# Kernel optimization log

Measured on AMD Instinct MI355X. Metric: run time of the kernel, lower is better.

Reference implementation:

```python
import jax, jax.numpy as jnp
import numpy as np

# sizes
N, B, NPG = 8192, 8, 1024          # total nodes, graphs, nodes per graph (equal-size graphs)
D, H, DH, L = 256, 8, 32, 2        # hidden, heads, head dim, layers
IN_C, OUT_D, E, DFF = 128, 64, 262144, 512
EPS = 1e-5


def setup_inputs() -> dict:
    key = jax.random.key(0)
    ks = jax.random.split(key, 20)
    p = lambda i, shp: jax.random.normal(ks[i], shp, jnp.float32) * 0.05
    return dict(
        x=jax.random.normal(ks[0], (N, IN_C), jnp.float32),
        edge_index=jax.random.randint(ks[1], (2, E), 0, N),
        batch=jnp.arange(N, dtype=jnp.int32) // NPG,  # sorted, equal-size graphs
        w_in=p(2, (D, IN_C)), b_in=p(3, (D,)),
        sage_wl=p(4, (L, D, D)), sage_bl=p(5, (L, D)), sage_wr=p(6, (L, D, D)),
        attn_iw=p(7, (L, 3 * D, D)), attn_ib=p(8, (L, 3 * D)),
        attn_ow=p(9, (L, D, D)), attn_ob=p(10, (L, D)),
        n1_w=jnp.ones((L, D)), n1_b=jnp.zeros((L, D)),
        n2_w=jnp.ones((L, D)), n2_b=jnp.zeros((L, D)),
        n3_w=jnp.ones((L, D)), n3_b=jnp.zeros((L, D)),
        mlp_w1=p(11, (L, DFF, D)), mlp_b1=p(12, (L, DFF)),
        mlp_w2=p(13, (L, D, DFF)), mlp_b2=p(14, (L, D)),
        bn_w=jnp.ones((L, D)), bn_b=jnp.zeros((L, D)),
        w_out=p(15, (OUT_D, D)), b_out=p(16, (OUT_D,)),
    )


def _bn(h, w, b):
    # BatchNorm1d over nodes (training-mode batch statistics, biased var)
    m = h.mean(0)
    v = jnp.mean((h - m) ** 2, axis=0)
    return (h - m) * jax.lax.rsqrt(v + EPS) * w + b


def _forward(x, edge_index, batch, w_in, b_in, sage_wl, sage_bl, sage_wr,
             attn_iw, attn_ib, attn_ow, attn_ob, n1_w, n1_b, n2_w, n2_b,
             n3_w, n3_b, mlp_w1, mlp_b1, mlp_w2, mlp_b2, bn_w, bn_b, w_out, b_out):
    src, dst = edge_index[0], edge_index[1]
    deg = jax.ops.segment_sum(jnp.ones((E,), jnp.float32), dst, num_segments=N)
    inv_deg = (1.0 / jnp.clip(deg, 1.0))[:, None]
    scale = 1.0 / np.sqrt(DH)

    h = x @ w_in.T + b_in  # in_proj Linear  [N, D]
    for l in range(L):
        # --- GPSConv: local SAGEConv (mean aggr) + residual + norm1 ---
        agg = jax.ops.segment_sum(h[src], dst, num_segments=N) * inv_deg
        loc = agg @ sage_wl[l].T + sage_bl[l] + h @ sage_wr[l].T
        loc = _bn(loc + h, n1_w[l], n1_b[l])
        # --- GPSConv: dense per-graph multi-head self-attention + residual + norm2 ---
        hd = h.reshape(B, NPG, D)  # to_dense_batch (no padding: equal graph sizes)
        qkv = hd @ attn_iw[l].T + attn_ib[l]  # [B, n, 3D]
        q, k, v = jnp.split(qkv, 3, axis=-1)
        sh = lambda t: t.reshape(B, NPG, H, DH).transpose(0, 2, 1, 3)  # [B, H, n, DH]
        a = jax.nn.softmax(jnp.einsum('bhqd,bhkd->bhqk', sh(q) * scale, sh(k)), axis=-1)
        o = jnp.einsum('bhqk,bhkd->bhqd', a, sh(v)).transpose(0, 2, 1, 3).reshape(B, NPG, D)
        o = (o @ attn_ow[l].T + attn_ob[l]).reshape(N, D)
        glob = _bn(o + h, n2_w[l], n2_b[l])
        # --- GPSConv: sum branches, MLP residual, norm3 ---
        out = loc + glob
        out = out + jax.nn.relu(out @ mlp_w1[l].T + mlp_b1[l]) @ mlp_w2[l].T + mlp_b2[l]
        out = _bn(out, n3_w[l], n3_b[l])
        # --- outer GPS: BatchNorm + relu + (dropout=eval) + residual ---
        h = h + jax.nn.relu(_bn(out, bn_w[l], bn_b[l]))
    pooled = h.reshape(B, NPG, D).mean(axis=1)  # global_mean_pool over sorted equal-size graphs
    return pooled @ w_out.T + b_out  # [B, OUT_D]


def reference(x, edge_index, batch, w_in, b_in, sage_wl, sage_bl, sage_wr,
              attn_iw, attn_ib, attn_ow, attn_ob, n1_w, n1_b, n2_w, n2_b,
              n3_w, n3_b, mlp_w1, mlp_b1, mlp_w2, mlp_b2, bn_w, bn_b, w_out, b_out):
    return _forward(x, edge_index, batch, w_in, b_in, sage_wl, sage_bl, sage_wr,
                    attn_iw, attn_ib, attn_ow, attn_ob, n1_w, n1_b, n2_w, n2_b,
                    n3_w, n3_b, mlp_w1, mlp_b1, mlp_w2, mlp_b2, bn_w, bn_b, w_out, b_out)
```

## Files before the change

kernel.cpp:

```cpp
#include <hip/hip_runtime.h>
#include <hip/hip_bf16.h>

#define N_NODES 8192
#define BGRAPH 8
#define NPG 1024
#define DIM 256
#define NH 8
#define DHEAD 32
#define NLAYERS 2
#define INC 128
#define OUTD 64
#define NEDGE 262144
#define DFF 512
#define EPS 1e-5f

typedef __attribute__((ext_vector_type(4))) float f32x4;
typedef __attribute__((ext_vector_type(8))) short s16x8;
typedef __attribute__((ext_vector_type(4))) ushort u16x4;

__device__ __forceinline__ float b2f(ushort u){
  unsigned v = ((unsigned)u) << 16;
  return __builtin_bit_cast(float, v);
}
__device__ __forceinline__ ushort f2b(float f){
  unsigned u = __builtin_bit_cast(unsigned, f);
  u += 0x7fffu + ((u >> 16) & 1u);
  return (ushort)(u >> 16);
}
__device__ __forceinline__ ushort f2b_trunc(float f){
  return (ushort)(__builtin_bit_cast(unsigned, f) >> 16);
}
__device__ __forceinline__ void gload16(const void* g, void* l){
  __builtin_amdgcn_global_load_lds(
    (const __attribute__((address_space(1))) void*)g,
    (__attribute__((address_space(3))) void*)l,
    16, 0, 0);
}

#define CX  1048576
#define CWI (CX+32768)
#define CSW (CWI+262144)
#define CIW (CSW+393216)
#define COW (CIW+131072)
#define CW1 (COW+262144)
#define CW2 (CW1+262144)
#define NCAST (CW2/256)
__global__ void k_setup(const float* __restrict__ x, const float* __restrict__ w_in,
    const float* __restrict__ wl, const float* __restrict__ wr,
    const float* __restrict__ iw, const float* __restrict__ ow,
    const float* __restrict__ w1, const float* __restrict__ w2,
    ushort* __restrict__ dst, const int* __restrict__ edst, int* __restrict__ deg){
  if(blockIdx.x >= NCAST){
    int i = (blockIdx.x - NCAST)*256 + threadIdx.x;
    int stride = 512*256;
    for(; i<NEDGE; i+=stride) atomicAdd(&deg[edst[i]], 1);
    return;
  }
  int i = blockIdx.x*256 + threadIdx.x;
  float val;
  if(i < CX)       val = x[i];
  else if(i < CWI) val = w_in[i-CX];
  else if(i < CSW){
    int j = i - CWI;
    int l = j >> 17, r = (j >> 9) & 255, k = j & 511;
    val = (k < 256) ? wl[(l<<16) + (r<<8) + k] : wr[(l<<16) + (r<<8) + (k-256)];
  }
  else if(i < CIW) val = iw[i-CSW];
  else if(i < COW) val = ow[i-CIW];
  else if(i < CW1) val = w1[i-COW];
  else             val = w2[i-CW1];
  dst[i] = f2b(val);
}

__global__ void k_scan(const int* __restrict__ deg, int* __restrict__ offs,
                       float* __restrict__ inv_deg){
  __shared__ int s[1024];
  int t = threadIdx.x;
  int base = t*8;
  int loc[8]; int acc=0;
  #pragma unroll
  for(int j=0;j<8;j++){
    int dv = deg[base+j];
    inv_deg[base+j] = 1.0f/(float)(dv>0?dv:1);
    loc[j]=acc; acc += dv;
  }
  s[t]=acc;
  __syncthreads();
  for(int d=1; d<1024; d<<=1){
    int v = (t>=d)? s[t-d] : 0;
    __syncthreads();
    if(t>=d) s[t]+=v;
    __syncthreads();
  }
  int pre = (t>0)? s[t-1] : 0;
  #pragma unroll
  for(int j=0;j<8;j++) offs[base+j] = pre + loc[j];
  if(t==1023) offs[N_NODES] = s[1023];
}
__global__ void k_fill_csr(const int* __restrict__ src, const int* __restrict__ dst,
                           const int* __restrict__ offs, int* __restrict__ cursor,
                           int* __restrict__ csr){
  int i = blockIdx.x*blockDim.x + threadIdx.x;
  int stride = gridDim.x*blockDim.x;
  for(; i<NEDGE; i+=stride){
    int d = dst[i];
    int p = atomicAdd(&cursor[d], 1);
    csr[offs[d]+p] = src[i];
  }
}

__global__ __launch_bounds__(256) void k_aggregate(ushort* __restrict__ hwb,
    const int* __restrict__ offs, const int* __restrict__ csr,
    const float* __restrict__ inv_deg){
  int n = blockIdx.x*4 + (threadIdx.x>>6);
  int lane = threadIdx.x & 63;
  int beg = offs[n], end = offs[n+1];
  f32x4 a0 = {0,0,0,0}, a1 = {0,0,0,0}, a2 = {0,0,0,0}, a3 = {0,0,0,0};
  int i = beg;
  for(; i+4<=end; i+=4){
    int j0=csr[i], j1=csr[i+1], j2=csr[i+2], j3=csr[i+3];
    u16x4 v0 = *(const u16x4*)(hwb + (size_t)j0*512 + 256 + lane*4);
    u16x4 v1 = *(const u16x4*)(hwb + (size_t)j1*512 + 256 + lane*4);
    u16x4 v2 = *(const u16x4*)(hwb + (size_t)j2*512 + 256 + lane*4);
    u16x4 v3 = *(const u16x4*)(hwb + (size_t)j3*512 + 256 + lane*4);
    #pragma unroll
    for(int c=0;c<4;c++){ a0[c]+=b2f(v0[c]); a1[c]+=b2f(v1[c]);
                          a2[c]+=b2f(v2[c]); a3[c]+=b2f(v3[c]); }
  }
  for(; i<end; ++i){
    int j0=csr[i];
    u16x4 v0 = *(const u16x4*)(hwb + (size_t)j0*512 + 256 + lane*4);
    #pragma unroll
    for(int c=0;c<4;c++) a0[c]+=b2f(v0[c]);
  }
  float inv = inv_deg[n];
  u16x4 outv;
  #pragma unroll
  for(int c=0;c<4;c++) outv[c] = f2b((a0[c]+a1[c]+a2[c]+a3[c])*inv);
  *(u16x4*)(hwb + (size_t)n*512 + lane*4) = outv;
}

#define STAGE_AB(t, buf) do{ \
    int kt_ = (t)*64; \
    _Pragma("unroll") \
    for(int it=0; it<2; ++it){ \
      int c = (wave*2+it)*64 + lane; \
      int row = c >> 3, q = c & 7; \
      int qs = q ^ (row & 7); \
      gload16(A + (size_t)(bm+row)*lda + kt_ + qs*8, (char*)As + (buf)*8192 + (wave*2+it)*1024); \
      gload16(W + (size_t)(bn+row)*K   + kt_ + qs*8, (char*)Bs + (buf)*8192 + (wave*2+it)*1024); \
    } \
  }while(0)

template<bool RELU, bool RESID, bool RESIDB, bool BIAS, bool WF32, bool WBF, bool STATS>
__global__ __launch_bounds__(256) void k_mm(const ushort* __restrict__ A,
    const ushort* __restrict__ W, const float* __restrict__ bias,
    const float* __restrict__ resid, const ushort* __restrict__ residb,
    float* __restrict__ Cf, ushort* __restrict__ Cb,
    float* __restrict__ gS, float* __restrict__ gQ,
    int M, int Nc, int K, int lda, int ldcb)
{
  __shared__ ushort As[2*64*64];
  __shared__ ushort Bs[2*64*64];
  __shared__ float sredS[64];
  __shared__ float sredQ[64];
  const int tid = threadIdx.x;
  const int lane = tid & 63, wave = tid >> 6;
  const int l15 = lane & 15, l4 = lane >> 4;
  const int bm = blockIdx.y*64, bn = blockIdx.x*64;
  const int wr = wave >> 1, wc = wave & 1;
  f32x4 acc[2][2] = {};
  const int nt = K >> 6;

  STAGE_AB(0, 0);
  asm volatile("s_waitcnt vmcnt(0)" ::: "memory");
  __builtin_amdgcn_s_barrier();

  int cur = 0;
  for(int t=0; t<nt; ++t){
    if(t+1 < nt) STAGE_AB(t+1, cur^1);
    #pragma unroll
    for(int kk=0; kk<2; ++kk){
      s16x8 af[2], bfr[2];
      #pragma unroll
      for(int mi=0; mi<2; ++mi){
        int row = wr*32 + mi*16 + l15;
        int col = (kk*64 + l4*16) ^ ((row & 7) << 4);
        af[mi] = *(const s16x8*)((const char*)As + cur*8192 + row*128 + col);
      }
      #pragma unroll
      for(int nj=0; nj<2; ++nj){
        int row = wc*32 + nj*16 + l15;
        int col = (kk*64 + l4*16) ^ ((row & 7) << 4);
        bfr[nj] = *(const s16x8*)((const char*)Bs + cur*8192 + row*128 + col);
      }
      #pragma unroll
      for(int mi=0; mi<2; ++mi)
        #pragma unroll
        for(int nj=0; nj<2; ++nj)
          acc[mi][nj] = __builtin_amdgcn_mfma_f32_16x16x32_bf16(af[mi], bfr[nj], acc[mi][nj], 0,0,0);
    }
    asm volatile("s_waitcnt vmcnt(0)" ::: "memory");
    __builtin_amdgcn_s_barrier();
    cur ^= 1;
  }

  float sloc[2] = {0.f,0.f}, qloc[2] = {0.f,0.f};
  #pragma unroll
  for(int mi=0; mi<2; ++mi){
    #pragma unroll
    for(int nj=0; nj<2; ++nj){
      int col = bn + wc*32 + nj*16 + l15;
      float bv = BIAS ? bias[col] : 0.f;
      #pragma unroll
      for(int r=0; r<4; ++r){
        int row = bm + wr*32 + mi*16 + l4*4 + r;
        size_t off = (size_t)row*Nc + col;
        float v = acc[mi][nj][r] + bv;
        if(RESID)  v += resid[off];
        if(RESIDB) v += b2f(residb[off]);
        if(RELU)   v = fmaxf(v, 0.f);
        if(WF32)   Cf[off] = v;
        if(WBF)    Cb[(size_t)row*ldcb + col] = f2b(v);
        if(STATS){ sloc[nj] += v; qloc[nj] += v*v; }
      }
    }
  }
  if(STATS){
    if(tid < 64){ sredS[tid]=0.f; sredQ[tid]=0.f; }
    __syncthreads();
    int c0 = wc*32 + l15;
    atomicAdd(&sredS[c0],    sloc[0]); atomicAdd(&sredQ[c0],    qloc[0]);
    atomicAdd(&sredS[c0+16], sloc[1]); atomicAdd(&sredQ[c0+16], qloc[1]);
    __syncthreads();
    if(tid < 64){
      atomicAdd(&gS[bn+tid], sredS[tid]);
      atomicAdd(&gQ[bn+tid], sredQ[tid]);
    }
  }
}

__global__ __launch_bounds__(256) void k_attn(const ushort* __restrict__ qkv,
                                              ushort* __restrict__ attnO)
{
  __shared__ ushort Ks[2][64*32];
  __shared__ ushort Vt[2][32*64];
  const int tid = threadIdx.x, lane = tid & 63, wave = tid >> 6;
  const int l15 = lane & 15, g = lane >> 4;
  int bid = blockIdx.x;
  int h  = bid & 7;
  int bg = (bid >> 3) & 7;
  int qc = bid >> 6;
  const int nb = bg*NPG + qc*64 + wave*16;
  const int kb = bg*NPG;

  const int rho = tid >> 2, qq = tid & 3;
  const int grp = rho >> 5, r32 = rho & 31;
  const int tt = r32 >> 4, wi = r32 & 15;
  const int jperm = grp*32 + (wi >> 2)*8 + tt*4 + (wi & 3);
  const int qs = qq ^ ((rho >> 1) & 3);

  s16x8 qf = *(const s16x8*)(qkv + (size_t)(nb + l15)*768 + h*32 + g*8);
  {
    const float scale2 = 0.2550370703637335f;
    #pragma unroll
    for(int i=0;i<8;i++) qf[i] = (short)f2b(b2f((ushort)qf[i]) * scale2);
  }
  f32x4 o0 = {0.f,0.f,0.f,0.f}, o1 = {0.f,0.f,0.f,0.f};
  float mrun = -1e30f, lrun = 0.f;

  gload16(qkv + (size_t)(kb + jperm)*768 + 256 + h*32 + qs*8, (char*)Ks[0] + wave*1024);
  s16x8 vcur = *(const s16x8*)(qkv + (size_t)(kb + lane)*768 + 512 + h*32 + wave*8);

  for(int st=0; st<16; ++st){
    int buf = st & 1;
    #pragma unroll
    for(int i=0;i<8;i++){
      int d = wave*8 + i;
      Vt[buf][d*64 + (lane ^ (i<<3))] = (ushort)vcur[i];
    }
    s16x8 vnext = vcur;
    if(st+1 < 16){
      gload16(qkv + (size_t)(kb + (st+1)*64 + jperm)*768 + 256 + h*32 + qs*8,
              (char*)Ks[buf^1] + wave*1024);
      vnext = *(const s16x8*)(qkv + (size_t)(kb + (st+1)*64 + lane)*768 + 512 + h*32 + wave*8);
      asm volatile("s_waitcnt vmcnt(2) lgkmcnt(0)" ::: "memory");
    } else {
      asm volatile("s_waitcnt vmcnt(0) lgkmcnt(0)" ::: "memory");
    }
    __builtin_amdgcn_s_barrier();

    f32x4 sc[4];
    __builtin_amdgcn_s_setprio(1);
    #pragma unroll
    for(int q4=0; q4<4; ++q4){
      int r0 = q4*16 + l15;
      s16x8 kf = *(const s16x8*)((const char*)Ks[buf] + r0*64 + ((g*16) ^ (((r0>>1)&3)<<4)));
      f32x4 z = {0.f,0.f,0.f,0.f};
      sc[q4] = __builtin_amdgcn_mfma_f32_16x16x32_bf16(kf, qf, z, 0,0,0);
    }
    __builtin_amdgcn_s_setprio(0);

    float smax = -1e30f;
    #pragma unroll
    for(int q4=0; q4<4; ++q4)
      #pragma unroll
      for(int r=0; r<4; ++r) smax = fmaxf(smax, sc[q4][r]);
    smax = fmaxf(smax, __shfl_xor(smax, 16));
    smax = fmaxf(smax, __shfl_xor(smax, 32));

    if(!__all((int)(smax <= mrun + 8.0f))){
      float mnew = fmaxf(mrun, smax);
      float alpha = exp2f(mrun - mnew);
      lrun *= alpha;
      #pragma unroll
      for(int r=0;r<4;r++){
        float ar = __shfl(alpha, (lane & 48) | (g*4 + r), 64);
        o0[r] *= ar; o1[r] *= ar;
      }
      mrun = mnew;
    }

    float p[16];
    float ps = 0.f;
    #pragma unroll
    for(int q4=0; q4<4; ++q4)
      #pragma unroll
      for(int r=0; r<4; ++r){
        float pv = exp2f(sc[q4][r] - mrun);
        p[q4*4+r] = pv; ps += pv;
      }
    ps += __shfl_xor(ps, 16);
    ps += __shfl_xor(ps, 32);
    lrun += ps;

    s16x8 pa0, pa1;
    #pragma unroll
    for(int i=0;i<8;i++){ pa0[i] = (short)f2b_trunc(p[i]); pa1[i] = (short)f2b_trunc(p[8+i]); }

    int colb0 = g*16, colb1 = 64 + g*16;
    int d0 = l15, d1 = l15 + 16;
    s16x8 v00 = *(const s16x8*)((const char*)Vt[buf] + d0*128 + (colb0 ^ ((d0&7)<<4)));
    s16x8 v01 = *(const s16x8*)((const char*)Vt[buf] + d1*128 + (colb0 ^ ((d1&7)<<4)));
    s16x8 v10 = *(const s16x8*)((const char*)Vt[buf] + d0*128 + (colb1 ^ ((d0&7)<<4)));
    s16x8 v11 = *(const s16x8*)((const char*)Vt[buf] + d1*128 + (colb1 ^ ((d1&7)<<4)));
    __builtin_amdgcn_s_setprio(1);
    o0 = __builtin_amdgcn_mfma_f32_16x16x32_bf16(pa0, v00, o0, 0,0,0);
    o1 = __builtin_amdgcn_mfma_f32_16x16x32_bf16(pa0, v01, o1, 0,0,0);
    o0 = __builtin_amdgcn_mfma_f32_16x16x32_bf16(pa1, v10, o0, 0,0,0);
    o1 = __builtin_amdgcn_mfma_f32_16x16x32_bf16(pa1, v11, o1, 0,0,0);
    __builtin_amdgcn_s_setprio(0);

    asm volatile("s_waitcnt lgkmcnt(0)" ::: "memory");
    __builtin_amdgcn_s_barrier();
    vcur = vnext;
  }
  float inv = 1.0f/lrun;
  #pragma unroll
  for(int r=0;r<4;r++){
    int q2 = g*4 + r;
    float ir = __shfl(inv, (lane & 48) | q2, 64);
    size_t nrow = (size_t)(nb + q2)*DIM + h*32;
    attnO[nrow + l15]      = f2b(o0[r]*ir);
    attnO[nrow + 16 + l15] = f2b(o1[r]*ir);
  }
}

__global__ __launch_bounds__(256) void k_apply12(const ushort* __restrict__ locB,
    const ushort* __restrict__ globB, const float* __restrict__ slot,
    const float* __restrict__ n1w, const float* __restrict__ n1b,
    const float* __restrict__ n2w, const float* __restrict__ n2b,
    ushort* __restrict__ combB){
  int d = threadIdx.x;
  size_t i = (size_t)blockIdx.x*DIM + d;
  const float invn = 1.0f/N_NODES;
  float m1 = slot[d]*invn,     v1 = slot[256+d]*invn - m1*m1;
  float m2 = slot[512+d]*invn, v2 = slot[768+d]*invn - m2*m2;
  float rs1 = rsqrtf(v1+EPS), rs2 = rsqrtf(v2+EPS);
  float y1 = (b2f(locB[i])-m1)*rs1*n1w[d] + n1b[d];
  float y2 = (b2f(globB[i])-m2)*rs2*n2w[d] + n2b[d];
  combB[i] = f2b(y1 + y2);
}

__global__ __launch_bounds__(256) void k_apply3o(const ushort* __restrict__ xB,
    const float* __restrict__ slot, const float* __restrict__ n3w,
    const float* __restrict__ n3b, const float* __restrict__ bw,
    const float* __restrict__ bb, float* __restrict__ H,
    ushort* __restrict__ hwbR){
  int d = threadIdx.x;
  size_t i = (size_t)blockIdx.x*DIM + d;
  const float invn = 1.0f/N_NODES;
  float m   = slot[1024+d]*invn;
  float var = slot[1280+d]*invn - m*m;
  float rs  = rsqrtf(var+EPS);
  float gch = rs*n3w[d];
  float rso = rsqrtf(gch*gch*var + EPS);
  float yo = (b2f(xB[i])-m)*gch*rso*bw[d] + bb[d];
  float h = H[i] + fmaxf(yo, 0.f);
  H[i] = h;
  hwbR[(size_t)blockIdx.x*512 + d] = f2b(h);
}

__global__ __launch_bounds__(256) void k_pool_out(const float* __restrict__ H,
    const float* __restrict__ w_out, const float* __restrict__ b_out,
    float* __restrict__ out){
  __shared__ float pl[256];
  int b = blockIdx.x, d = threadIdx.x;
  float s = 0.f;
  const float* base = H + (size_t)b*NPG*DIM + d;
  for(int r=0; r<NPG; ++r) s += base[(size_t)r*DIM];
  pl[d] = s * (1.0f/NPG);
  __syncthreads();
  if(d < OUTD){
    float acc = b_out[d];
    #pragma unroll 4
    for(int k=0; k<DIM; ++k) acc += pl[k]*w_out[d*DIM+k];
    out[b*OUTD + d] = acc;
  }
}

extern "C" void kernel_launch(void* const* d_in, const int* in_sizes, int n_in,
                              void* d_out, int out_size, void* d_ws, size_t ws_size,
                              hipStream_t stream) {
  const float* x       = (const float*)d_in[0];
  const int*   edge    = (const int*)d_in[1];
  const float* w_in    = (const float*)d_in[3];
  const float* b_in    = (const float*)d_in[4];
  const float* sage_wl = (const float*)d_in[5];
  const float* sage_bl = (const float*)d_in[6];
  const float* sage_wr = (const float*)d_in[7];
  const float* attn_iw = (const float*)d_in[8];
  const float* attn_ib = (const float*)d_in[9];
  const float* attn_ow = (const float*)d_in[10];
  const float* attn_ob = (const float*)d_in[11];
  const float* n1_w = (const float*)d_in[12];
  const float* n1_b = (const float*)d_in[13];
  const float* n2_w = (const float*)d_in[14];
  const float* n2_b = (const float*)d_in[15];
  const float* n3_w = (const float*)d_in[16];
  const float* n3_b = (const float*)d_in[17];
  const float* mlp_w1 = (const float*)d_in[18];
  const float* mlp_b1 = (const float*)d_in[19];
  const float* mlp_w2 = (const float*)d_in[20];
  const float* mlp_b2 = (const float*)d_in[21];
  const float* bn_w = (const float*)d_in[22];
  const float* bn_b = (const float*)d_in[23];
  const float* w_out = (const float*)d_in[24];
  const float* b_out = (const float*)d_in[25];

  const size_t ND = (size_t)N_NODES*DIM;
  float* ws    = (float*)d_ws;
  float* H     = ws;
  ushort* wsb   = (ushort*)(ws + ND);
  ushort* locB  = wsb;
  ushort* globB = wsb + ND;
  ushort* hwb   = wsb + 2*ND;
  ushort* qkvb  = wsb + 4*ND;
  ushort* attnOb= wsb + 7*ND;
  ushort* combb = wsb + 8*ND;
  ushort* hidb  = wsb + 9*ND;
  ushort* castb = wsb + 11*ND;
  ushort* xb     = castb;
  ushort* w_in_b = castb + CX;
  ushort* sageWb = castb + CWI;
  ushort* iw_b   = castb + CSW;
  ushort* ow_b   = castb + CIW;
  ushort* w1_b   = castb + COW;
  ushort* w2_b   = castb + CW1;
  float* mf      = (float*)(castb + CW2);
  float* inv_deg = mf;
  float* bnslots = mf + 8192;
  int* deg    = (int*)(bnslots + 3072);
  int* cursor = deg + N_NODES;
  int* offs   = cursor + N_NODES;
  int* csr    = offs + N_NODES + 8;

  const int* esrc = edge;
  const int* edst = edge + NEDGE;

  hipMemsetAsync(bnslots, 0, 3072*sizeof(float) + 2*N_NODES*sizeof(int), stream);

  k_setup<<<NCAST+512,256,0,stream>>>(x, w_in, sage_wl, sage_wr, attn_iw,
      attn_ow, mlp_w1, mlp_w2, castb, edst, deg);
  k_scan<<<1,1024,0,stream>>>(deg, offs, inv_deg);
  k_fill_csr<<<512,256,0,stream>>>(esrc, edst, offs, cursor, csr);

  k_mm<false,false,false,true,true,true,false><<<dim3(4,128),256,0,stream>>>(
      xb, w_in_b, b_in, nullptr, nullptr, H, hwb+256, nullptr, nullptr,
      N_NODES, DIM, INC, INC, 512);

  for(int l=0; l<NLAYERS; ++l){
    const ushort* swb = sageWb + (size_t)l*131072;
    const ushort* iwb = iw_b + (size_t)l*196608;
    const ushort* owb = ow_b + (size_t)l*65536;
    const ushort* w1b = w1_b + (size_t)l*131072;
    const ushort* w2b = w2_b + (size_t)l*131072;
    float* slot = bnslots + (size_t)l*1536;

    k_aggregate<<<N_NODES/4,256,0,stream>>>(hwb, offs, csr, inv_deg);
    k_mm<false,true,false,true,false,true,true><<<dim3(4,128),256,0,stream>>>(
        hwb, swb, sage_bl + l*DIM, H, nullptr, nullptr, locB, slot, slot+256,
        N_NODES, DIM, 512, 512, DIM);

    k_mm<false,false,false,true,false,true,false><<<dim3(12,128),256,0,stream>>>(
        hwb+256, iwb, attn_ib + l*3*DIM, nullptr, nullptr, nullptr, qkvb,
        nullptr, nullptr, N_NODES, 3*DIM, DIM, 512, 768);
    k_attn<<<1024,256,0,stream>>>(qkvb, attnOb);
    k_mm<false,true,false,true,false,true,true><<<dim3(4,128),256,0,stream>>>(
        attnOb, owb, attn_ob + l*DIM, H, nullptr, nullptr, globB, slot+512, slot+768,
        N_NODES, DIM, DIM, DIM, DIM);

    k_apply12<<<N_NODES,256,0,stream>>>(locB, globB, slot,
        n1_w + l*DIM, n1_b + l*DIM, n2_w + l*DIM, n2_b + l*DIM, combb);

    k_mm<true,false,false,true,false,true,false><<<dim3(8,128),256,0,stream>>>(
        combb, w1b, mlp_b1 + l*DFF, nullptr, nullptr, nullptr, hidb,
        nullptr, nullptr, N_NODES, DFF, DIM, DIM, 512);
    k_mm<false,false,true,true,false,true,true><<<dim3(4,128),256,0,stream>>>(
        hidb, w2b, mlp_b2 + l*DIM, nullptr, combb, nullptr, globB,
        slot+1024, slot+1280, N_NODES, DIM, 512, 512, DIM);

    k_apply3o<<<N_NODES,256,0,stream>>>(globB, slot, n3_w + l*DIM, n3_b + l*DIM,
        bn_w + l*DIM, bn_b + l*DIM, H, hwb+256);
  }

  k_pool_out<<<BGRAPH,256,0,stream>>>(H, w_out, b_out, (float*)d_out);
}
```

Baseline: 320.4 us.

## Fuse SAGE linear and QKV projection into one GEMM with zero-padded weights

Concatenates the SAGE weights and the QKV in-projection weights into a single 1024x512 bf16 matrix. The QKV rows are zero-padded over the aggregated half of K, so one launch computes both outputs from the shared [agg|h] input. The epilogue branches on column block: SAGE blocks add the residual and accumulate BN stats, while QKV blocks write qkv. This saves a kernel launch and a re-read of h, but the QKV part now does twice the K work on zeros.

```diff
diff --git a/kernel.cpp b/kernel.cpp
--- a/kernel.cpp
+++ b/kernel.cpp
@@ -39,9 +39,8 @@
 
 #define CX  1048576
 #define CWI (CX+32768)
-#define CSW (CWI+262144)
-#define CIW (CSW+393216)
-#define COW (CIW+131072)
+#define CSQ (CWI+1048576)
+#define COW (CSQ+131072)
 #define CW1 (COW+262144)
 #define CW2 (CW1+262144)
 #define NCAST (CW2/256)
@@ -60,13 +59,16 @@
   float val;
   if(i < CX)       val = x[i];
   else if(i < CWI) val = w_in[i-CX];
-  else if(i < CSW){
+  else if(i < CSQ){
     int j = i - CWI;
-    int l = j >> 17, r = (j >> 9) & 255, k = j & 511;
-    val = (k < 256) ? wl[(l<<16) + (r<<8) + k] : wr[(l<<16) + (r<<8) + (k-256)];
-  }
-  else if(i < CIW) val = iw[i-CSW];
-  else if(i < COW) val = ow[i-CIW];
+    int l = j >> 19, rk = j & 524287;
+    int r = rk >> 9, k = rk & 511;
+    if(r < 256)
+      val = (k < 256) ? wl[l*65536 + r*256 + k] : wr[l*65536 + r*256 + (k-256)];
+    else
+      val = (k < 256) ? 0.f : iw[((size_t)l*768 + (r-256))*256 + (k-256)];
+  }
+  else if(i < COW) val = ow[i-CSQ];
   else if(i < CW1) val = w1[i-COW];
   else             val = w2[i-CW1];
   dst[i] = f2b(val);
@@ -151,6 +153,41 @@
       gload16(W + (size_t)(bn+row)*K   + kt_ + qs*8, (char*)Bs + (buf)*8192 + (wave*2+it)*1024); \
     } \
   }while(0)
+
+#define MM_CORE \
+  f32x4 acc[2][2] = {}; \
+  const int nt = K >> 6; \
+  STAGE_AB(0, 0); \
+  asm volatile("s_waitcnt vmcnt(0)" ::: "memory"); \
+  __builtin_amdgcn_s_barrier(); \
+  int cur = 0; \
+  for(int t=0; t<nt; ++t){ \
+    if(t+1 < nt) STAGE_AB(t+1, cur^1); \
+    _Pragma("unroll") \
+    for(int kk=0; kk<2; ++kk){ \
+      s16x8 af[2], bfr[2]; \
+      _Pragma("unroll") \
+      for(int mi=0; mi<2; ++mi){ \
+        int row = wr*32 + mi*16 + l15; \
+        int col = (kk*64 + l4*16) ^ ((row & 7) << 4); \
+        af[mi] = *(const s16x8*)((const char*)As + cur*8192 + row*128 + col); \
+      } \
+      _Pragma("unroll") \
+      for(int nj=0; nj<2; ++nj){ \
+        int row = wc*32 + nj*16 + l15; \
+        int col = (kk*64 + l4*16) ^ ((row & 7) << 4); \
+        bfr[nj] = *(const s16x8*)((const char*)Bs + cur*8192 + row*128 + col); \
+      } \
+      _Pragma("unroll") \
+      for(int mi=0; mi<2; ++mi) \
+        _Pragma("unroll") \
+        for(int nj=0; nj<2; ++nj) \
+          acc[mi][nj] = __builtin_amdgcn_mfma_f32_16x16x32_bf16(af[mi], bfr[nj], acc[mi][nj], 0,0,0); \
+    } \
+    asm volatile("s_waitcnt vmcnt(0)" ::: "memory"); \
+    __builtin_amdgcn_s_barrier(); \
+    cur ^= 1; \
+  }
 
 template<bool RELU, bool RESID, bool RESIDB, bool BIAS, bool WF32, bool WBF, bool STATS>
 __global__ __launch_bounds__(256) void k_mm(const ushort* __restrict__ A,
@@ -169,41 +206,7 @@
   const int l15 = lane & 15, l4 = lane >> 4;
   const int bm = blockIdx.y*64, bn = blockIdx.x*64;
   const int wr = wave >> 1, wc = wave & 1;
-  f32x4 acc[2][2] = {};
-  const int nt = K >> 6;
-
-  STAGE_AB(0, 0);
-  asm volatile("s_waitcnt vmcnt(0)" ::: "memory");
-  __builtin_amdgcn_s_barrier();
-
-  int cur = 0;
-  for(int t=0; t<nt; ++t){
-    if(t+1 < nt) STAGE_AB(t+1, cur^1);
-    #pragma unroll
-    for(int kk=0; kk<2; ++kk){
-      s16x8 af[2], bfr[2];
-      #pragma unroll
-      for(int mi=0; mi<2; ++mi){
-        int row = wr*32 + mi*16 + l15;
-        int col = (kk*64 + l4*16) ^ ((row & 7) << 4);
-        af[mi] = *(const s16x8*)((const char*)As + cur*8192 + row*128 + col);
-      }
-      #pragma unroll
-      for(int nj=0; nj<2; ++nj){
-        int row = wc*32 + nj*16 + l15;
-        int col = (kk*64 + l4*16) ^ ((row & 7) << 4);
-        bfr[nj] = *(const s16x8*)((const char*)Bs + cur*8192 + row*128 + col);
-      }
-      #pragma unroll
-      for(int mi=0; mi<2; ++mi)
-        #pragma unroll
-        for(int nj=0; nj<2; ++nj)
-          acc[mi][nj] = __builtin_amdgcn_mfma_f32_16x16x32_bf16(af[mi], bfr[nj], acc[mi][nj], 0,0,0);
-    }
-    asm volatile("s_waitcnt vmcnt(0)" ::: "memory");
-    __builtin_amdgcn_s_barrier();
-    cur ^= 1;
-  }
+  MM_CORE
 
   float sloc[2] = {0.f,0.f}, qloc[2] = {0.f,0.f};
   #pragma unroll
@@ -227,6 +230,60 @@
     }
   }
   if(STATS){
+    if(tid < 64){ sredS[tid]=0.f; sredQ[tid]=0.f; }
+    __syncthreads();
+    int c0 = wc*32 + l15;
+    atomicAdd(&sredS[c0],    sloc[0]); atomicAdd(&sredQ[c0],    qloc[0]);
+    atomicAdd(&sredS[c0+16], sloc[1]); atomicAdd(&sredQ[c0+16], qloc[1]);
+    __syncthreads();
+    if(tid < 64){
+      atomicAdd(&gS[bn+tid], sredS[tid]);
+      atomicAdd(&gQ[bn+tid], sredQ[tid]);
+    }
+  }
+}
+
+__global__ __launch_bounds__(256) void k_mm_sq(const ushort* __restrict__ A,
+    const ushort* __restrict__ W, const float* __restrict__ sage_bl,
+    const float* __restrict__ attn_ib, const float* __restrict__ H,
+    ushort* __restrict__ locB, ushort* __restrict__ qkvb,
+    float* __restrict__ gS, float* __restrict__ gQ)
+{
+  __shared__ ushort As[2*64*64];
+  __shared__ ushort Bs[2*64*64];
+  __shared__ float sredS[64];
+  __shared__ float sredQ[64];
+  const int tid = threadIdx.x;
+  const int lane = tid & 63, wave = tid >> 6;
+  const int l15 = lane & 15, l4 = lane >> 4;
+  const int bm = blockIdx.y*64, bn = blockIdx.x*64;
+  const int wr = wave >> 1, wc = wave & 1;
+  const int K = 512, lda = 512;
+  MM_CORE
+
+  const bool sage = (bn < 256);
+  float sloc[2] = {0.f,0.f}, qloc[2] = {0.f,0.f};
+  #pragma unroll
+  for(int mi=0; mi<2; ++mi){
+    #pragma unroll
+    for(int nj=0; nj<2; ++nj){
+      int col = bn + wc*32 + nj*16 + l15;
+      float bv = sage ? sage_bl[col] : attn_ib[col-256];
+      #pragma unroll
+      for(int r=0; r<4; ++r){
+        int row = bm + wr*32 + mi*16 + l4*4 + r;
+        float v = acc[mi][nj][r] + bv;
+        if(sage){
+          v += H[(size_t)row*DIM + col];
+          locB[(size_t)row*DIM + col] = f2b(v);
+          sloc[nj] += v; qloc[nj] += v*v;
+        } else {
+          qkvb[(size_t)row*768 + (col-256)] = f2b(v);
+        }
+      }
+    }
+  }
+  if(sage){
     if(tid < 64){ sredS[tid]=0.f; sredQ[tid]=0.f; }
     __syncthreads();
     int c0 = wc*32 + l15;
@@ -462,9 +519,8 @@
   ushort* castb = wsb + 11*ND;
   ushort* xb     = castb;
   ushort* w_in_b = castb + CX;
-  ushort* sageWb = castb + CWI;
-  ushort* iw_b   = castb + CSW;
-  ushort* ow_b   = castb + CIW;
+  ushort* sqw_b  = castb + CWI;
+  ushort* ow_b   = castb + CSQ;
   ushort* w1_b   = castb + COW;
   ushort* w2_b   = castb + CW1;
   float* mf      = (float*)(castb + CW2);
@@ -490,21 +546,16 @@
       N_NODES, DIM, INC, INC, 512);
 
   for(int l=0; l<NLAYERS; ++l){
-    const ushort* swb = sageWb + (size_t)l*131072;
-    const ushort* iwb = iw_b + (size_t)l*196608;
+    const ushort* sqb = sqw_b + (size_t)l*524288;
     const ushort* owb = ow_b + (size_t)l*65536;
     const ushort* w1b = w1_b + (size_t)l*131072;
     const ushort* w2b = w2_b + (size_t)l*131072;
     float* slot = bnslots + (size_t)l*1536;
 
     k_aggregate<<<N_NODES/4,256,0,stream>>>(hwb, offs, csr, inv_deg);
-    k_mm<false,true,false,true,false,true,true><<<dim3(4,128),256,0,stream>>>(
-        hwb, swb, sage_bl + l*DIM, H, nullptr, nullptr, locB, slot, slot+256,
-        N_NODES, DIM, 512, 512, DIM);
-
-    k_mm<false,false,false,true,false,true,false><<<dim3(12,128),256,0,stream>>>(
-        hwb+256, iwb, attn_ib + l*3*DIM, nullptr, nullptr, nullptr, qkvb,
-        nullptr, nullptr, N_NODES, 3*DIM, DIM, 512, 768);
+    k_mm_sq<<<dim3(16,128),256,0,stream>>>(hwb, sqb, sage_bl + l*DIM,
+        attn_ib + l*3*DIM, H, locB, qkvb, slot, slot+256);
+
     k_attn<<<1024,256,0,stream>>>(qkvb, attnOb);
     k_mm<false,true,false,true,false,true,true><<<dim3(4,128),256,0,stream>>>(
         attnOb, owb, attn_ob + l*DIM, H, nullptr, nullptr, globB, slot+512, slot+768,
```

After: 343.0 us. 7.1% more time.
